# Optimization experiments

Measured on AMD Instinct MI355X. Metric: run time of the kernel, lower is better.

Reference implementation:

```python
import jax, jax.numpy as jnp
import numpy as np

FFT_BINS = 513   # win_length//2 + 1
WIN = 1024       # win_length
H = 128          # LSTM hidden size (both blocks)
ENC = 256        # encoder_size
EPS = 1e-7


def _lstm_cell(x, h, c, Wih, Whh, bih, bhh):
    # x: [1, in], h/c: [1, H]; PyTorch gate order i, f, g, o
    g = x @ Wih.T + bih + h @ Whh.T + bhh
    i, f, gg, o = jnp.split(g, 4, axis=-1)
    c2 = jax.nn.sigmoid(f) * c + jax.nn.sigmoid(i) * jnp.tanh(gg)
    h2 = jax.nn.sigmoid(o) * jnp.tanh(c2)
    return h2, c2


def _sep_block(x, states, Wih0, Whh0, bih0, bhh0, Wih1, Whh1, bih1, bhh1, dw, db):
    # x: [1,1,in]; states: [1,1,2*2*H] -> [2(h/c), 2(layers), 1, H]
    st = states.reshape(2, 2, 1, H)
    h0, c0 = st[0], st[1]
    xt = x[:, 0]                                   # [1, in]
    h1, c1 = _lstm_cell(xt, h0[0], c0[0], Wih0, Whh0, bih0, bhh0)
    h2, c2 = _lstm_cell(h1, h0[1], c0[1], Wih1, Whh1, bih1, bhh1)
    mask = jax.nn.sigmoid(h2 @ dw.T + db)[:, None, :]   # [1,1,in]
    out_states = jnp.stack([jnp.stack([h1, h2]), jnp.stack([c1, c2])]).reshape(1, 1, -1)
    return mask, out_states


def setup_inputs() -> dict:
    key = jax.random.key(0)
    ks = jax.random.split(key, 32)
    s = 0.08  # ~ 1/sqrt(H), matching PyTorch LSTM init scale
    def n(i, shape, sc=s):
        return jax.random.normal(ks[i], shape, dtype=jnp.float32) * sc
    inp = {
        "mag": jax.random.uniform(ks[0], (1, 1, FFT_BINS), dtype=jnp.float32),
        "phase": n(1, (1, 1, FFT_BINS), 3.0),
        "in_states1": n(2, (1, 1, 2 * 2 * H), 1.0),
        "in_states2": n(3, (1, 1, 2 * 2 * H), 1.0),
        # sep1 LSTM (input 513)
        "w_ih1_0": n(4, (4 * H, FFT_BINS)), "w_hh1_0": n(5, (4 * H, H)),
        "b_ih1_0": n(6, (4 * H,)), "b_hh1_0": n(7, (4 * H,)),
        "w_ih1_1": n(8, (4 * H, H)), "w_hh1_1": n(9, (4 * H, H)),
        "b_ih1_1": n(10, (4 * H,)), "b_hh1_1": n(11, (4 * H,)),
        "dense1_w": n(12, (FFT_BINS, H)), "dense1_b": n(13, (FFT_BINS,)),
        # encoder 1x1 conv (no bias) + instant layernorm
        "enc_w": n(14, (ENC, WIN)),
        "gamma": jnp.ones((1, 1, ENC), jnp.float32),
        "beta": jnp.zeros((1, 1, ENC), jnp.float32),
        # sep2 LSTM (input 256)
        "w_ih2_0": n(15, (4 * H, ENC)), "w_hh2_0": n(16, (4 * H, H)),
        "b_ih2_0": n(17, (4 * H,)), "b_hh2_0": n(18, (4 * H,)),
        "w_ih2_1": n(19, (4 * H, H)), "w_hh2_1": n(20, (4 * H, H)),
        "b_ih2_1": n(21, (4 * H,)), "b_hh2_1": n(22, (4 * H,)),
        "dense2_w": n(23, (ENC, H)), "dense2_b": n(24, (ENC,)),
        # decoder 1x1 conv (no bias)
        "dec_w": n(25, (WIN, ENC)),
    }
    return inp


def reference(mag, phase, in_states1, in_states2,
              w_ih1_0, w_hh1_0, b_ih1_0, b_hh1_0,
              w_ih1_1, w_hh1_1, b_ih1_1, b_hh1_1,
              dense1_w, dense1_b, enc_w, gamma, beta,
              w_ih2_0, w_hh2_0, b_ih2_0, b_hh2_0,
              w_ih2_1, w_hh2_1, b_ih2_1, b_hh2_1,
              dense2_w, dense2_b, dec_w):
    # Branch 1: magnitude masking in STFT domain
    mask1, out_states1 = _sep_block(mag, in_states1, w_ih1_0, w_hh1_0, b_ih1_0,
                                    b_hh1_0, w_ih1_1, w_hh1_1, b_ih1_1, b_hh1_1,
                                    dense1_w, dense1_b)
    est_mag = mask1 * mag
    s1_stft = est_mag * jnp.exp(1j * phase)          # [1,1,513] complex64
    y1 = jnp.fft.irfft(s1_stft, axis=-1)             # [1,1,1024]
    # encoder 1x1 conv (permute + conv1d(k=1) == matmul over channels)
    enc = jnp.einsum('btw,ew->bte', y1, enc_w)       # [1,1,256]
    # instant layer norm over channels
    mean = jnp.mean(enc, axis=-1, keepdims=True)
    var = jnp.mean(jnp.square(enc - mean), axis=-1, keepdims=True)
    enc_norm = (enc - mean) / jnp.sqrt(var + EPS) * gamma + beta
    # Branch 2: learned-domain masking
    mask2, out_states2 = _sep_block(enc_norm, in_states2, w_ih2_0, w_hh2_0,
                                    b_ih2_0, b_hh2_0, w_ih2_1, w_hh2_1,
                                    b_ih2_1, b_hh2_1, dense2_w, dense2_b)
    est_enc = mask2 * enc
    decoded = jnp.einsum('bte,we->bwt', est_enc, dec_w)  # [1,1024,1]
    return decoded, out_states1, out_states2
```

## Files before the change

### kernel.cpp

```cpp
#include <hip/hip_runtime.h>
#include <hip/hip_bf16.h>


#define HDIM 128
#define NBLK 128
typedef __hip_bfloat16 bf16;

__device__ float G[4608];
#define O_H1A 0
#define O_H2A 128
#define O_C1A 256
#define O_C2A 384
#define O_H1B 512
#define O_H2B 640
#define O_C1B 768
#define O_C2B 896
#define O_XR  1024
#define O_XI  1600
#define O_Y   2176
#define O_ENC 3200
#define O_EST 3456

__device__ __forceinline__ float gld(int i) {
    return __hip_atomic_load(&G[i], __ATOMIC_RELAXED, __HIP_MEMORY_SCOPE_AGENT);
}
__device__ __forceinline__ void gst(int i, float v) {
    __hip_atomic_store(&G[i], v, __ATOMIC_RELAXED, __HIP_MEMORY_SCOPE_AGENT);
}

__device__ unsigned g_flags[NBLK * 16];

struct Smem {
    float tc[1024], ts[1024];
    float xn[256];
    float g4[4];
    float red[4];
    unsigned base;
};

__device__ __forceinline__ void gridbar(const Smem& s, int b, unsigned j) {
    __syncthreads();
    if (threadIdx.x == 0)
        __hip_atomic_store(&g_flags[b * 16], s.base + j, __ATOMIC_RELEASE,
                           __HIP_MEMORY_SCOPE_AGENT);
    if (threadIdx.x < NBLK) {
        const unsigned tgt = s.base + j;
        while ((int)(__hip_atomic_load(&g_flags[threadIdx.x * 16],
                                       __ATOMIC_RELAXED,
                                       __HIP_MEMORY_SCOPE_AGENT) - tgt) < 0) {}
    }
    __syncthreads();
}

__device__ __forceinline__ bool is_bf(const void* probe) {
    return (((const unsigned*)probe)[0] & 0xFFFFu) == 0x3F80u;
}
template <bool BF>
__device__ __forceinline__ float ldin(const void* p, int i) {
    return BF ? __bfloat162float(((const bf16*)p)[i]) : ((const float*)p)[i];
}
template <bool BF>
__device__ __forceinline__ void stout(void* p, int i, float v) {
    if (BF) ((bf16*)p)[i] = __float2bfloat16(v);
    else    ((float*)p)[i] = v;
}
__device__ __forceinline__ float wred(float v) {
#pragma unroll
    for (int m = 32; m; m >>= 1) v += __shfl_xor(v, m);
    return v;
}
__device__ __forceinline__ float sigm(float x) { return 1.f / (1.f + expf(-x)); }

struct Params {
    const void *mag, *phase, *st1, *st2;
    const void *wih10, *whh10, *bih10, *bhh10;
    const void *wih11, *whh11, *bih11, *bhh11;
    const void *d1w, *d1b, *encw, *gamma, *beta;
    const void *wih20, *whh20, *bih20, *bhh20;
    const void *wih21, *whh21, *bih21, *bhh21;
    const void *d2w, *d2b, *decw;
    void *out;
};

template <bool BF>
__device__ void body(const Params& p, Smem& s)
{
    const int tid  = threadIdx.x, lane = tid & 63, wave = tid >> 6;
    const int b    = blockIdx.x;
    const int wgid = b * 4 + wave;
    const int row  = wave * HDIM + b;

    if (tid == 0)
        s.base = __hip_atomic_load(&g_flags[b * 16], __ATOMIC_RELAXED,
                                   __HIP_MEMORY_SCOPE_AGENT);

    for (int i = tid; i < 1024; i += 256) {
        float th = (float)i * (6.283185307179586f / 1024.f);
        sincosf(th, &s.ts[i], &s.tc[i]);
    }

    float a_w[8], a_x[8], a_wh[2], a_h[2];
#pragma unroll
    for (int i = 0; i < 8; ++i) {
        const int k = lane + 64 * i;
        a_w[i] = ldin<BF>(p.wih10, row * 513 + k);
        a_x[i] = ldin<BF>(p.mag, k);
    }
    float a_w512 = 0.f, a_x512 = 0.f;
    if (lane == 0) {
        a_w512 = ldin<BF>(p.wih10, row * 513 + 512);
        a_x512 = ldin<BF>(p.mag, 512);
    }
#pragma unroll
    for (int i = 0; i < 2; ++i) {
        const int k = lane + 64 * i;
        a_wh[i] = ldin<BF>(p.whh10, row * HDIM + k);
        a_h[i]  = ldin<BF>(p.st1, k);
    }
    float a_bi = ldin<BF>(p.bih10, row), a_bh = ldin<BF>(p.bhh10, row);
    float a_c  = ldin<BF>(p.st1, 256 + b);
    float b_w[2], b_wh[2], b_h[2];
#pragma unroll
    for (int i = 0; i < 2; ++i) {
        const int k = lane + 64 * i;
        b_w[i]  = ldin<BF>(p.wih11, row * HDIM + k);
        b_wh[i] = ldin<BF>(p.whh11, row * HDIM + k);
        b_h[i]  = ldin<BF>(p.st1, 128 + k);
    }
    float b_bi = ldin<BF>(p.bih11, row), b_bh = ldin<BF>(p.bhh11, row);
    float b_c  = ldin<BF>(p.st1, 384 + b);
    float c_w0[2], c_w1[2] = {0.f, 0.f};
#pragma unroll
    for (int i = 0; i < 2; ++i)
        c_w0[i] = ldin<BF>(p.d1w, wgid * HDIM + lane + 64 * i);
    float c_b0 = ldin<BF>(p.d1b, wgid);
    float c_m0 = ldin<BF>(p.mag, wgid);
    float c_p0 = ldin<BF>(p.phase, wgid);
    float c_b1 = 0.f, c_m1 = 0.f, c_p1 = 0.f;
    if (wgid == 0) {
#pragma unroll
        for (int i = 0; i < 2; ++i)
            c_w1[i] = ldin<BF>(p.d1w, 512 * HDIM + lane + 64 * i);
        c_b1 = ldin<BF>(p.d1b, 512);
        c_m1 = ldin<BF>(p.mag, 512);
        c_p1 = ldin<BF>(p.phase, 512);
    }
    float e_w[16];
    if (wgid < 256) {
#pragma unroll
        for (int i = 0; i < 16; ++i)
            e_w[i] = ldin<BF>(p.encw, wgid * 1024 + lane + 64 * i);
    }
    float f_w[4], f_wh[2], f_h[2];
#pragma unroll
    for (int i = 0; i < 4; ++i)
        f_w[i] = ldin<BF>(p.wih20, row * 256 + lane + 64 * i);
#pragma unroll
    for (int i = 0; i < 2; ++i) {
        const int k = lane + 64 * i;
        f_wh[i] = ldin<BF>(p.whh20, row * HDIM + k);
        f_h[i]  = ldin<BF>(p.st2, k);
    }
    float f_bi = ldin<BF>(p.bih20, row), f_bh = ldin<BF>(p.bhh20, row);
    float f_c  = ldin<BF>(p.st2, 256 + b);
    float f_g  = ldin<BF>(p.gamma, tid), f_be = ldin<BF>(p.beta, tid);
    float g_w[2], g_wh[2], g_h[2];
#pragma unroll
    for (int i = 0; i < 2; ++i) {
        const int k = lane + 64 * i;
        g_w[i]  = ldin<BF>(p.wih21, row * HDIM + k);
        g_wh[i] = ldin<BF>(p.whh21, row * HDIM + k);
        g_h[i]  = ldin<BF>(p.st2, 128 + k);
    }
    float g_bi = ldin<BF>(p.bih21, row), g_bh = ldin<BF>(p.bhh21, row);
    float g_c  = ldin<BF>(p.st2, 384 + b);
    float h_w[2] = {0.f, 0.f}, h_b = 0.f;
    if (wgid < 256) {
#pragma unroll
        for (int i = 0; i < 2; ++i)
            h_w[i] = ldin<BF>(p.d2w, wgid * HDIM + lane + 64 * i);
        h_b = ldin<BF>(p.d2b, wgid);
    }
    float i_w0[4], i_w1[4];
#pragma unroll
    for (int i = 0; i < 4; ++i) {
        i_w0[i] = ldin<BF>(p.decw, wgid * 256 + lane + 64 * i);
        i_w1[i] = ldin<BF>(p.decw, (wgid + 512) * 256 + lane + 64 * i);
    }

    {
        float acc = 0.f;
#pragma unroll
        for (int i = 0; i < 8; ++i) acc += a_w[i] * a_x[i];
        if (lane == 0) acc += a_w512 * a_x512;
#pragma unroll
        for (int i = 0; i < 2; ++i) acc += a_wh[i] * a_h[i];
        acc = wred(acc);
        if (lane == 0) s.g4[wave] = acc + a_bi + a_bh;
    }
    __syncthreads();
    if (tid == 0) {
        float c2 = sigm(s.g4[1]) * a_c + sigm(s.g4[0]) * tanhf(s.g4[2]);
        gst(O_H1A + b, sigm(s.g4[3]) * tanhf(c2));
        gst(O_C1A + b, c2);
    }
    gridbar(s, b, 1);

    {
        float x0 = gld(O_H1A + lane), x1 = gld(O_H1A + 64 + lane);
        float acc = b_w[0] * x0 + b_w[1] * x1;
#pragma unroll
        for (int i = 0; i < 2; ++i) acc += b_wh[i] * b_h[i];
        acc = wred(acc);
        if (lane == 0) s.g4[wave] = acc + b_bi + b_bh;
    }
    __syncthreads();
    if (tid == 0) {
        float c2 = sigm(s.g4[1]) * b_c + sigm(s.g4[0]) * tanhf(s.g4[2]);
        gst(O_H2A + b, sigm(s.g4[3]) * tanhf(c2));
        gst(O_C2A + b, c2);
    }
    gridbar(s, b, 2);

    {
        float h0 = gld(O_H2A + lane), h1 = gld(O_H2A + 64 + lane);
        {
            float acc = c_w0[0] * h0 + c_w0[1] * h1;
            acc = wred(acc);
            if (lane == 0) {
                float m = sigm(acc + c_b0);
                float em = m * c_m0;
                float sp, cp;
                sincosf(c_p0, &sp, &cp);
                gst(O_XR + wgid, em * cp);
                gst(O_XI + wgid, em * sp);
            }
        }
        if (wgid == 0) {
            float acc = c_w1[0] * h0 + c_w1[1] * h1;
            acc = wred(acc);
            if (lane == 0) {
                float m = sigm(acc + c_b1);
                float em = m * c_m1;
                float sp, cp;
                sincosf(c_p1, &sp, &cp);
                gst(O_XR + 512, em * cp);
                gst(O_XI + 512, em * sp);
            }
        }
    }
    if (b == 0) {
        for (int t = tid; t < 512; t += 256) stout<BF>(p.out, 1024 + t, gld(t));
    }
    gridbar(s, b, 3);

    {
        float dxr[8], dxi[8];
#pragma unroll
        for (int i = 0; i < 8; ++i) {
            const int k = lane + 64 * i;
            dxr[i] = gld(O_XR + k);
            dxi[i] = gld(O_XI + k);
        }
        float dxr512 = (lane == 0) ? gld(O_XR + 512) : 0.f;
#pragma unroll
        for (int r = 0; r < 2; ++r) {
            const int n = wgid + r * 512;
            float acc = 0.f;
            if (lane == 0) {
                acc += dxr[0];
            } else {
                int m = (lane * n) & 1023;
                acc += 2.f * (dxr[0] * s.tc[m] - dxi[0] * s.ts[m]);
            }
#pragma unroll
            for (int i = 1; i < 8; ++i) {
                const int k = lane + 64 * i;
                int m = (k * n) & 1023;
                acc += 2.f * (dxr[i] * s.tc[m] - dxi[i] * s.ts[m]);
            }
            if (lane == 0) acc += (n & 1) ? -dxr512 : dxr512;
            acc = wred(acc);
            if (lane == 0) gst(O_Y + n, acc * (1.f / 1024.f));
        }
    }
    gridbar(s, b, 4);

    if (wgid < 256) {
        float acc = 0.f;
#pragma unroll
        for (int i = 0; i < 16; ++i)
            acc += e_w[i] * gld(O_Y + lane + 64 * i);
        acc = wred(acc);
        if (lane == 0) gst(O_ENC + wgid, acc);
    }
    gridbar(s, b, 5);

    {
        float v = gld(O_ENC + tid);
        float sm = wred(v);
        if (lane == 0) s.red[wave] = sm;
        __syncthreads();
        float mean = (s.red[0] + s.red[1] + s.red[2] + s.red[3]) * (1.f / 256.f);
        __syncthreads();
        float d = v - mean;
        float s2 = wred(d * d);
        if (lane == 0) s.red[wave] = s2;
        __syncthreads();
        float var = (s.red[0] + s.red[1] + s.red[2] + s.red[3]) * (1.f / 256.f);
        float rs = rsqrtf(var + 1e-7f);
        s.xn[tid] = d * rs * f_g + f_be;
        __syncthreads();
        float acc = 0.f;
#pragma unroll
        for (int i = 0; i < 4; ++i) acc += f_w[i] * s.xn[lane + 64 * i];
#pragma unroll
        for (int i = 0; i < 2; ++i) acc += f_wh[i] * f_h[i];
        acc = wred(acc);
        if (lane == 0) s.g4[wave] = acc + f_bi + f_bh;
        __syncthreads();
        if (tid == 0) {
            float c2 = sigm(s.g4[1]) * f_c + sigm(s.g4[0]) * tanhf(s.g4[2]);
            gst(O_H1B + b, sigm(s.g4[3]) * tanhf(c2));
            gst(O_C1B + b, c2);
        }
    }
    gridbar(s, b, 6);

    {
        float x0 = gld(O_H1B + lane), x1 = gld(O_H1B + 64 + lane);
        float acc = g_w[0] * x0 + g_w[1] * x1;
#pragma unroll
        for (int i = 0; i < 2; ++i) acc += g_wh[i] * g_h[i];
        acc = wred(acc);
        if (lane == 0) s.g4[wave] = acc + g_bi + g_bh;
    }
    __syncthreads();
    if (tid == 0) {
        float c2 = sigm(s.g4[1]) * g_c + sigm(s.g4[0]) * tanhf(s.g4[2]);
        gst(O_H2B + b, sigm(s.g4[3]) * tanhf(c2));
        gst(O_C2B + b, c2);
    }
    gridbar(s, b, 7);

    if (wgid < 256) {
        float encv = gld(O_ENC + wgid);
        float h0 = gld(O_H2B + lane), h1 = gld(O_H2B + 64 + lane);
        float acc = h_w[0] * h0 + h_w[1] * h1;
        acc = wred(acc);
        if (lane == 0) {
            float m = sigm(acc + h_b);
            gst(O_EST + wgid, m * encv);
        }
    }
    if (b == 0) {
        for (int t = tid; t < 512; t += 256) stout<BF>(p.out, 1536 + t, gld(512 + t));
    }
    gridbar(s, b, 8);

    {
        float e0 = gld(O_EST + lane),       e1 = gld(O_EST + 64 + lane);
        float e2 = gld(O_EST + 128 + lane), e3 = gld(O_EST + 192 + lane);
        {
            float acc = i_w0[0] * e0 + i_w0[1] * e1 + i_w0[2] * e2 + i_w0[3] * e3;
            acc = wred(acc);
            if (lane == 0) stout<BF>(p.out, wgid, acc);
        }
        {
            float acc = i_w1[0] * e0 + i_w1[1] * e1 + i_w1[2] * e2 + i_w1[3] * e3;
            acc = wred(acc);
            if (lane == 0) stout<BF>(p.out, wgid + 512, acc);
        }
    }
}

__global__ __launch_bounds__(256, 1) void k_fused(Params p)
{
    __shared__ Smem s;
    if (is_bf(p.gamma)) body<true>(p, s);
    else                body<false>(p, s);
}

extern "C" void kernel_launch(void* const* d_in, const int* in_sizes, int n_in,
                              void* d_out, int out_size, void* d_ws, size_t ws_size,
                              hipStream_t stream)
{
    Params hp;
    hp.mag   = d_in[0];  hp.phase = d_in[1];  hp.st1 = d_in[2];  hp.st2 = d_in[3];
    hp.wih10 = d_in[4];  hp.whh10 = d_in[5];  hp.bih10 = d_in[6];  hp.bhh10 = d_in[7];
    hp.wih11 = d_in[8];  hp.whh11 = d_in[9];  hp.bih11 = d_in[10]; hp.bhh11 = d_in[11];
    hp.d1w   = d_in[12]; hp.d1b   = d_in[13]; hp.encw  = d_in[14];
    hp.gamma = d_in[15]; hp.beta  = d_in[16];
    hp.wih20 = d_in[17]; hp.whh20 = d_in[18]; hp.bih20 = d_in[19]; hp.bhh20 = d_in[20];
    hp.wih21 = d_in[21]; hp.whh21 = d_in[22]; hp.bih21 = d_in[23]; hp.bhh21 = d_in[24];
    hp.d2w   = d_in[25]; hp.d2b   = d_in[26]; hp.decw  = d_in[27];
    hp.out   = d_out;

    hipLaunchKernelGGL(k_fused, dim3(NBLK), dim3(256), 0, stream, hp);
}
```

Measured before the change: 142.5 us.

## Split grid barrier into arrive/wait and overlap weight loads with first barrier

The grid barrier is split into separate arrive and wait phases. The first LSTM cell is now computed right after its own weights load, and the block arrives at the barrier before loading the remaining weights and building the twiddle table, so those loads and sincos work overlap the barrier wait. Block 0's state-output copies are moved between arrive and wait, and the spin loop now calls s_sleep to reduce polling contention on the flags. The sleep may add some wake-up latency to each barrier.

```diff
diff --git a/kernel.cpp b/kernel.cpp
--- a/kernel.cpp
+++ b/kernel.cpp
@@ -38,16 +38,19 @@
     unsigned base;
 };
 
-__device__ __forceinline__ void gridbar(const Smem& s, int b, unsigned j) {
+__device__ __forceinline__ void bar_arrive(const Smem& s, int b, unsigned j) {
     __syncthreads();
     if (threadIdx.x == 0)
         __hip_atomic_store(&g_flags[b * 16], s.base + j, __ATOMIC_RELEASE,
                            __HIP_MEMORY_SCOPE_AGENT);
+}
+__device__ __forceinline__ void bar_wait(const Smem& s, unsigned j) {
     if (threadIdx.x < NBLK) {
         const unsigned tgt = s.base + j;
         while ((int)(__hip_atomic_load(&g_flags[threadIdx.x * 16],
                                        __ATOMIC_RELAXED,
-                                       __HIP_MEMORY_SCOPE_AGENT) - tgt) < 0) {}
+                                       __HIP_MEMORY_SCOPE_AGENT) - tgt) < 0)
+            __builtin_amdgcn_s_sleep(1);
     }
     __syncthreads();
 }
@@ -94,11 +97,6 @@
         s.base = __hip_atomic_load(&g_flags[b * 16], __ATOMIC_RELAXED,
                                    __HIP_MEMORY_SCOPE_AGENT);
 
-    for (int i = tid; i < 1024; i += 256) {
-        float th = (float)i * (6.283185307179586f / 1024.f);
-        sincosf(th, &s.ts[i], &s.tc[i]);
-    }
-
     float a_w[8], a_x[8], a_wh[2], a_h[2];
 #pragma unroll
     for (int i = 0; i < 8; ++i) {
@@ -119,6 +117,25 @@
     }
     float a_bi = ldin<BF>(p.bih10, row), a_bh = ldin<BF>(p.bhh10, row);
     float a_c  = ldin<BF>(p.st1, 256 + b);
+
+    {
+        float acc = 0.f;
+#pragma unroll
+        for (int i = 0; i < 8; ++i) acc += a_w[i] * a_x[i];
+        if (lane == 0) acc += a_w512 * a_x512;
+#pragma unroll
+        for (int i = 0; i < 2; ++i) acc += a_wh[i] * a_h[i];
+        acc = wred(acc);
+        if (lane == 0) s.g4[wave] = acc + a_bi + a_bh;
+    }
+    __syncthreads();
+    if (tid == 0) {
+        float c2 = sigm(s.g4[1]) * a_c + sigm(s.g4[0]) * tanhf(s.g4[2]);
+        gst(O_H1A + b, sigm(s.g4[3]) * tanhf(c2));
+        gst(O_C1A + b, c2);
+    }
+    bar_arrive(s, b, 1);
+
     float b_w[2], b_wh[2], b_h[2];
 #pragma unroll
     for (int i = 0; i < 2; ++i) {
@@ -187,24 +204,12 @@
         i_w0[i] = ldin<BF>(p.decw, wgid * 256 + lane + 64 * i);
         i_w1[i] = ldin<BF>(p.decw, (wgid + 512) * 256 + lane + 64 * i);
     }
-
-    {
-        float acc = 0.f;
-#pragma unroll
-        for (int i = 0; i < 8; ++i) acc += a_w[i] * a_x[i];
-        if (lane == 0) acc += a_w512 * a_x512;
-#pragma unroll
-        for (int i = 0; i < 2; ++i) acc += a_wh[i] * a_h[i];
-        acc = wred(acc);
-        if (lane == 0) s.g4[wave] = acc + a_bi + a_bh;
-    }
-    __syncthreads();
-    if (tid == 0) {
-        float c2 = sigm(s.g4[1]) * a_c + sigm(s.g4[0]) * tanhf(s.g4[2]);
-        gst(O_H1A + b, sigm(s.g4[3]) * tanhf(c2));
-        gst(O_C1A + b, c2);
-    }
-    gridbar(s, b, 1);
+    for (int i = tid; i < 1024; i += 256) {
+        float th = (float)i * (6.283185307179586f / 1024.f);
+        sincosf(th, &s.ts[i], &s.tc[i]);
+    }
+    asm volatile("" ::: "memory");
+    bar_wait(s, 1);
 
     {
         float x0 = gld(O_H1A + lane), x1 = gld(O_H1A + 64 + lane);
@@ -220,7 +225,8 @@
         gst(O_H2A + b, sigm(s.g4[3]) * tanhf(c2));
         gst(O_C2A + b, c2);
     }
-    gridbar(s, b, 2);
+    bar_arrive(s, b, 2);
+    bar_wait(s, 2);
 
     {
         float h0 = gld(O_H2A + lane), h1 = gld(O_H2A + 64 + lane);
@@ -249,10 +255,11 @@
             }
         }
     }
+    bar_arrive(s, b, 3);
     if (b == 0) {
         for (int t = tid; t < 512; t += 256) stout<BF>(p.out, 1024 + t, gld(t));
     }
-    gridbar(s, b, 3);
+    bar_wait(s, 3);
 
     {
         float dxr[8], dxi[8];
@@ -284,7 +291,8 @@
             if (lane == 0) gst(O_Y + n, acc * (1.f / 1024.f));
         }
     }
-    gridbar(s, b, 4);
+    bar_arrive(s, b, 4);
+    bar_wait(s, 4);
 
     if (wgid < 256) {
         float acc = 0.f;
@@ -294,7 +302,8 @@
         acc = wred(acc);
         if (lane == 0) gst(O_ENC + wgid, acc);
     }
-    gridbar(s, b, 5);
+    bar_arrive(s, b, 5);
+    bar_wait(s, 5);
 
     {
         float v = gld(O_ENC + tid);
@@ -325,7 +334,8 @@
             gst(O_C1B + b, c2);
         }
     }
-    gridbar(s, b, 6);
+    bar_arrive(s, b, 6);
+    bar_wait(s, 6);
 
     {
         float x0 = gld(O_H1B + lane), x1 = gld(O_H1B + 64 + lane);
@@ -341,7 +351,8 @@
         gst(O_H2B + b, sigm(s.g4[3]) * tanhf(c2));
         gst(O_C2B + b, c2);
     }
-    gridbar(s, b, 7);
+    bar_arrive(s, b, 7);
+    bar_wait(s, 7);
 
     if (wgid < 256) {
         float encv = gld(O_ENC + wgid);
@@ -353,10 +364,11 @@
             gst(O_EST + wgid, m * encv);
         }
     }
+    bar_arrive(s, b, 8);
     if (b == 0) {
         for (int t = tid; t < 512; t += 256) stout<BF>(p.out, 1536 + t, gld(512 + t));
     }
-    gridbar(s, b, 8);
+    bar_wait(s, 8);
 
     {
         float e0 = gld(O_EST + lane),       e1 = gld(O_EST + 64 + lane);
```

Measured after the change: 139.5 us. -2.1%, faster.

## Replace grid barriers with epoch-tagged dataflow polling on packed values

Applied to the files above, without the earlier changes.

Replaces all eight grid-wide flag barriers with per-value 64-bit slots that pack a per-launch epoch tag next to the float payload. Consumers spin only on the specific values they need, which lets blocks proceed as soon as their inputs are ready rather than waiting for the slowest block. The first LSTM cell is also computed and posted before the remaining weights are loaded, and the twiddle table is built after those loads to overlap latency. The epoch is read and bumped per block per launch, which relies on every block running the same number of launches. The spin loops add global polling traffic.

```diff
diff --git a/kernel.cpp b/kernel.cpp
--- a/kernel.cpp
+++ b/kernel.cpp
@@ -6,7 +6,7 @@
 #define NBLK 128
 typedef __hip_bfloat16 bf16;
 
-__device__ float G[4608];
+__device__ unsigned long long GT[4608];
 #define O_H1A 0
 #define O_H2A 128
 #define O_C1A 256
@@ -21,35 +21,33 @@
 #define O_ENC 3200
 #define O_EST 3456
 
-__device__ __forceinline__ float gld(int i) {
-    return __hip_atomic_load(&G[i], __ATOMIC_RELAXED, __HIP_MEMORY_SCOPE_AGENT);
-}
-__device__ __forceinline__ void gst(int i, float v) {
-    __hip_atomic_store(&G[i], v, __ATOMIC_RELAXED, __HIP_MEMORY_SCOPE_AGENT);
-}
-
-__device__ unsigned g_flags[NBLK * 16];
-
-struct Smem {
-    float tc[1024], ts[1024];
-    float xn[256];
-    float g4[4];
-    float red[4];
-    unsigned base;
-};
-
-__device__ __forceinline__ void gridbar(const Smem& s, int b, unsigned j) {
-    __syncthreads();
-    if (threadIdx.x == 0)
-        __hip_atomic_store(&g_flags[b * 16], s.base + j, __ATOMIC_RELEASE,
-                           __HIP_MEMORY_SCOPE_AGENT);
-    if (threadIdx.x < NBLK) {
-        const unsigned tgt = s.base + j;
-        while ((int)(__hip_atomic_load(&g_flags[threadIdx.x * 16],
-                                       __ATOMIC_RELAXED,
-                                       __HIP_MEMORY_SCOPE_AGENT) - tgt) < 0) {}
-    }
-    __syncthreads();
+__device__ unsigned g_epoch[NBLK * 16];
+
+__device__ __forceinline__ void postf(int i, float v, unsigned ep) {
+    union { float f; unsigned u; } c; c.f = v;
+    __hip_atomic_store(&GT[i], ((unsigned long long)ep << 32) | c.u,
+                       __ATOMIC_RELAXED, __HIP_MEMORY_SCOPE_AGENT);
+}
+template <int N>
+__device__ __forceinline__ void pollS(int base, int stride, unsigned ep,
+                                      float* out) {
+    unsigned long long w[N];
+    bool ok;
+    do {
+        ok = true;
+#pragma unroll
+        for (int j = 0; j < N; ++j)
+            w[j] = __hip_atomic_load(&GT[base + j * stride], __ATOMIC_RELAXED,
+                                     __HIP_MEMORY_SCOPE_AGENT);
+#pragma unroll
+        for (int j = 0; j < N; ++j)
+            ok &= ((unsigned)(w[j] >> 32) == ep);
+    } while (!ok);
+#pragma unroll
+    for (int j = 0; j < N; ++j) {
+        union { unsigned u; float f; } c; c.u = (unsigned)w[j];
+        out[j] = c.f;
+    }
 }
 
 __device__ __forceinline__ bool is_bf(const void* probe) {
@@ -82,6 +80,14 @@
     void *out;
 };
 
+struct Smem {
+    float tc[1024], ts[1024];
+    float xn[256];
+    float g4[4];
+    float red[4];
+    unsigned ep;
+};
+
 template <bool BF>
 __device__ void body(const Params& p, Smem& s)
 {
@@ -90,13 +96,12 @@
     const int wgid = b * 4 + wave;
     const int row  = wave * HDIM + b;
 
-    if (tid == 0)
-        s.base = __hip_atomic_load(&g_flags[b * 16], __ATOMIC_RELAXED,
-                                   __HIP_MEMORY_SCOPE_AGENT);
-
-    for (int i = tid; i < 1024; i += 256) {
-        float th = (float)i * (6.283185307179586f / 1024.f);
-        sincosf(th, &s.ts[i], &s.tc[i]);
+    if (tid == 0) {
+        unsigned e = __hip_atomic_load(&g_epoch[b * 16], __ATOMIC_RELAXED,
+                                       __HIP_MEMORY_SCOPE_AGENT) + 1u;
+        __hip_atomic_store(&g_epoch[b * 16], e, __ATOMIC_RELAXED,
+                           __HIP_MEMORY_SCOPE_AGENT);
+        s.ep = e;
     }
 
     float a_w[8], a_x[8], a_wh[2], a_h[2];
@@ -119,6 +124,25 @@
     }
     float a_bi = ldin<BF>(p.bih10, row), a_bh = ldin<BF>(p.bhh10, row);
     float a_c  = ldin<BF>(p.st1, 256 + b);
+
+    {
+        float acc = 0.f;
+#pragma unroll
+        for (int i = 0; i < 8; ++i) acc += a_w[i] * a_x[i];
+        if (lane == 0) acc += a_w512 * a_x512;
+#pragma unroll
+        for (int i = 0; i < 2; ++i) acc += a_wh[i] * a_h[i];
+        acc = wred(acc);
+        if (lane == 0) s.g4[wave] = acc + a_bi + a_bh;
+    }
+    __syncthreads();
+    const unsigned ep = s.ep;
+    if (tid == 0) {
+        float c2 = sigm(s.g4[1]) * a_c + sigm(s.g4[0]) * tanhf(s.g4[2]);
+        postf(O_H1A + b, sigm(s.g4[3]) * tanhf(c2), ep);
+        postf(O_C1A + b, c2, ep);
+    }
+
     float b_w[2], b_wh[2], b_h[2];
 #pragma unroll
     for (int i = 0; i < 2; ++i) {
@@ -187,28 +211,16 @@
         i_w0[i] = ldin<BF>(p.decw, wgid * 256 + lane + 64 * i);
         i_w1[i] = ldin<BF>(p.decw, (wgid + 512) * 256 + lane + 64 * i);
     }
-
-    {
-        float acc = 0.f;
-#pragma unroll
-        for (int i = 0; i < 8; ++i) acc += a_w[i] * a_x[i];
-        if (lane == 0) acc += a_w512 * a_x512;
-#pragma unroll
-        for (int i = 0; i < 2; ++i) acc += a_wh[i] * a_h[i];
-        acc = wred(acc);
-        if (lane == 0) s.g4[wave] = acc + a_bi + a_bh;
-    }
-    __syncthreads();
-    if (tid == 0) {
-        float c2 = sigm(s.g4[1]) * a_c + sigm(s.g4[0]) * tanhf(s.g4[2]);
-        gst(O_H1A + b, sigm(s.g4[3]) * tanhf(c2));
-        gst(O_C1A + b, c2);
-    }
-    gridbar(s, b, 1);
-
-    {
-        float x0 = gld(O_H1A + lane), x1 = gld(O_H1A + 64 + lane);
-        float acc = b_w[0] * x0 + b_w[1] * x1;
+    for (int i = tid; i < 1024; i += 256) {
+        float th = (float)i * (6.283185307179586f / 1024.f);
+        sincosf(th, &s.ts[i], &s.tc[i]);
+    }
+    asm volatile("" ::: "memory");
+
+    {
+        float x01[2];
+        pollS<2>(O_H1A + lane, 64, ep, x01);
+        float acc = b_w[0] * x01[0] + b_w[1] * x01[1];
 #pragma unroll
         for (int i = 0; i < 2; ++i) acc += b_wh[i] * b_h[i];
         acc = wred(acc);
@@ -217,52 +229,51 @@
     __syncthreads();
     if (tid == 0) {
         float c2 = sigm(s.g4[1]) * b_c + sigm(s.g4[0]) * tanhf(s.g4[2]);
-        gst(O_H2A + b, sigm(s.g4[3]) * tanhf(c2));
-        gst(O_C2A + b, c2);
-    }
-    gridbar(s, b, 2);
-
-    {
-        float h0 = gld(O_H2A + lane), h1 = gld(O_H2A + 64 + lane);
+        postf(O_H2A + b, sigm(s.g4[3]) * tanhf(c2), ep);
+        postf(O_C2A + b, c2, ep);
+    }
+
+    {
+        float h01[2];
+        pollS<2>(O_H2A + lane, 64, ep, h01);
         {
-            float acc = c_w0[0] * h0 + c_w0[1] * h1;
+            float acc = c_w0[0] * h01[0] + c_w0[1] * h01[1];
             acc = wred(acc);
             if (lane == 0) {
                 float m = sigm(acc + c_b0);
                 float em = m * c_m0;
                 float sp, cp;
                 sincosf(c_p0, &sp, &cp);
-                gst(O_XR + wgid, em * cp);
-                gst(O_XI + wgid, em * sp);
+                postf(O_XR + wgid, em * cp, ep);
+                postf(O_XI + wgid, em * sp, ep);
             }
         }
         if (wgid == 0) {
-            float acc = c_w1[0] * h0 + c_w1[1] * h1;
+            float acc = c_w1[0] * h01[0] + c_w1[1] * h01[1];
             acc = wred(acc);
             if (lane == 0) {
                 float m = sigm(acc + c_b1);
                 float em = m * c_m1;
                 float sp, cp;
                 sincosf(c_p1, &sp, &cp);
-                gst(O_XR + 512, em * cp);
-                gst(O_XI + 512, em * sp);
+                postf(O_XR + 512, em * cp, ep);
+                postf(O_XI + 512, em * sp, ep);
             }
         }
     }
     if (b == 0) {
-        for (int t = tid; t < 512; t += 256) stout<BF>(p.out, 1024 + t, gld(t));
-    }
-    gridbar(s, b, 3);
+        float sv[2];
+        pollS<2>(tid, 256, ep, sv);
+        stout<BF>(p.out, 1024 + tid, sv[0]);
+        stout<BF>(p.out, 1024 + tid + 256, sv[1]);
+    }
 
     {
         float dxr[8], dxi[8];
-#pragma unroll
-        for (int i = 0; i < 8; ++i) {
-            const int k = lane + 64 * i;
-            dxr[i] = gld(O_XR + k);
-            dxi[i] = gld(O_XI + k);
-        }
-        float dxr512 = (lane == 0) ? gld(O_XR + 512) : 0.f;
+        pollS<8>(O_XR + lane, 64, ep, dxr);
+        pollS<8>(O_XI + lane, 64, ep, dxi);
+        float dxr512 = 0.f;
+        if (lane == 0) pollS<1>(O_XR + 512, 0, ep, &dxr512);
 #pragma unroll
         for (int r = 0; r < 2; ++r) {
             const int n = wgid + r * 512;
@@ -281,23 +292,23 @@
             }
             if (lane == 0) acc += (n & 1) ? -dxr512 : dxr512;
             acc = wred(acc);
-            if (lane == 0) gst(O_Y + n, acc * (1.f / 1024.f));
-        }
-    }
-    gridbar(s, b, 4);
+            if (lane == 0) postf(O_Y + n, acc * (1.f / 1024.f), ep);
+        }
+    }
 
     if (wgid < 256) {
+        float yv[16];
+        pollS<16>(O_Y + lane, 64, ep, yv);
         float acc = 0.f;
 #pragma unroll
-        for (int i = 0; i < 16; ++i)
-            acc += e_w[i] * gld(O_Y + lane + 64 * i);
-        acc = wred(acc);
-        if (lane == 0) gst(O_ENC + wgid, acc);
-    }
-    gridbar(s, b, 5);
-
-    {
-        float v = gld(O_ENC + tid);
+        for (int i = 0; i < 16; ++i) acc += e_w[i] * yv[i];
+        acc = wred(acc);
+        if (lane == 0) postf(O_ENC + wgid, acc, ep);
+    }
+
+    {
+        float v;
+        pollS<1>(O_ENC + tid, 0, ep, &v);
         float sm = wred(v);
         if (lane == 0) s.red[wave] = sm;
         __syncthreads();
@@ -321,15 +332,15 @@
         __syncthreads();
         if (tid == 0) {
             float c2 = sigm(s.g4[1]) * f_c + sigm(s.g4[0]) * tanhf(s.g4[2]);
-            gst(O_H1B + b, sigm(s.g4[3]) * tanhf(c2));
-            gst(O_C1B + b, c2);
-        }
-    }
-    gridbar(s, b, 6);
-
-    {
-        float x0 = gld(O_H1B + lane), x1 = gld(O_H1B + 64 + lane);
-        float acc = g_w[0] * x0 + g_w[1] * x1;
+            postf(O_H1B + b, sigm(s.g4[3]) * tanhf(c2), ep);
+            postf(O_C1B + b, c2, ep);
+        }
+    }
+
+    {
+        float x01[2];
+        pollS<2>(O_H1B + lane, 64, ep, x01);
+        float acc = g_w[0] * x01[0] + g_w[1] * x01[1];
 #pragma unroll
         for (int i = 0; i < 2; ++i) acc += g_wh[i] * g_h[i];
         acc = wred(acc);
@@ -338,36 +349,41 @@
     __syncthreads();
     if (tid == 0) {
         float c2 = sigm(s.g4[1]) * g_c + sigm(s.g4[0]) * tanhf(s.g4[2]);
-        gst(O_H2B + b, sigm(s.g4[3]) * tanhf(c2));
-        gst(O_C2B + b, c2);
-    }
-    gridbar(s, b, 7);
+        postf(O_H2B + b, sigm(s.g4[3]) * tanhf(c2), ep);
+        postf(O_C2B + b, c2, ep);
+    }
 
     if (wgid < 256) {
-        float encv = gld(O_ENC + wgid);
-        float h0 = gld(O_H2B + lane), h1 = gld(O_H2B + 64 + lane);
-        float acc = h_w[0] * h0 + h_w[1] * h1;
+        float encv;
+        pollS<1>(O_ENC + wgid, 0, ep, &encv);
+        float h01[2];
+        pollS<2>(O_H2B + lane, 64, ep, h01);
+        float acc = h_w[0] * h01[0] + h_w[1] * h01[1];
         acc = wred(acc);
         if (lane == 0) {
             float m = sigm(acc + h_b);
-            gst(O_EST + wgid, m * encv);
+            postf(O_EST + wgid, m * encv, ep);
         }
     }
     if (b == 0) {
-        for (int t = tid; t < 512; t += 256) stout<BF>(p.out, 1536 + t, gld(512 + t));
-    }
-    gridbar(s, b, 8);
-
-    {
-        float e0 = gld(O_EST + lane),       e1 = gld(O_EST + 64 + lane);
-        float e2 = gld(O_EST + 128 + lane), e3 = gld(O_EST + 192 + lane);
+        float sv[2];
+        pollS<2>(512 + tid, 256, ep, sv);
+        stout<BF>(p.out, 1536 + tid, sv[0]);
+        stout<BF>(p.out, 1536 + tid + 256, sv[1]);
+    }
+
+    {
+        float e4[4];
+        pollS<4>(O_EST + lane, 64, ep, e4);
         {
-            float acc = i_w0[0] * e0 + i_w0[1] * e1 + i_w0[2] * e2 + i_w0[3] * e3;
+            float acc = i_w0[0] * e4[0] + i_w0[1] * e4[1] +
+                        i_w0[2] * e4[2] + i_w0[3] * e4[3];
             acc = wred(acc);
             if (lane == 0) stout<BF>(p.out, wgid, acc);
         }
         {
-            float acc = i_w1[0] * e0 + i_w1[1] * e1 + i_w1[2] * e2 + i_w1[3] * e3;
+            float acc = i_w1[0] * e4[0] + i_w1[1] * e4[1] +
+                        i_w1[2] * e4[2] + i_w1[3] * e4[3];
             acc = wred(acc);
             if (lane == 0) stout<BF>(p.out, wgid + 512, acc);
         }
```

Result: faster. 136.6 us (-4.1%).
